# Kernel tuning notes

Hardware: AMD Instinct MI355X
Metric: run time of the kernel (lower is better)

## Reference

```python
import jax, jax.numpy as jnp
import numpy as np

N_NODES = 50000
N_EDGES = 800000  # avg degree 16
D = 16            # in_features == out_features (required by final matmul shape)


def setup_inputs() -> dict:
    key = jax.random.key(0)
    k1, k2, k3, k4 = jax.random.split(key, 4)
    x = jax.random.normal(k1, (N_NODES, D), dtype=jnp.float32)
    edge_index = jax.random.randint(k2, (2, N_EDGES), 0, N_NODES, dtype=jnp.int64)
    # shared internal weight of the (0e x 0e -> 0e, 'uvw') segmented tensor product
    W_tp = jax.random.normal(k3, (D, D, D), dtype=jnp.float32) * (1.0 / D)
    # nn.Parameter(torch.randn(out, in) * 0.01)
    weight = jax.random.normal(k4, (D, D), dtype=jnp.float32) * 0.01
    bias = jnp.zeros((D,), dtype=jnp.float32)
    return {"x": x, "edge_index": edge_index, "W_tp": W_tp, "weight": weight, "bias": bias}


def reference(x, edge_index, W_tp, weight, bias):
    # x: [N, D]; edge_index: [2, E]
    row, col = edge_index[0], edge_index[1]
    xr = x[row]  # gather source-node features   [E, D]
    xc = x[col]  # gather neighbor-node features [E, D]
    # Equivariant tensor product: with greedy irreps everything lands in 0e,
    # the only CG-allowed path is 0e x 0e -> 0e with CG coeff 1 and a shared
    # fully-connected ('uvw') weight -> per-edge bilinear form.
    messages = jnp.einsum('eu,ev,uvw->ew', xr, xc, W_tp)  # [E, D]
    # scatter-add messages back to the row nodes (index_add_)
    out = jnp.zeros((x.shape[0], D), dtype=x.dtype).at[row].add(messages)
    # dense linear: out @ weight.T + bias
    return out @ weight.T + bias
```

## Files before the change

### kernel.cpp

```cpp
#include <hip/hip_runtime.h>
#include <hip/hip_bf16.h>


#define D16 16
#define WF_STRIDE 260

__global__ __launch_bounds__(256) void fuse_w(const float* __restrict__ Wtp,
                                              const float* __restrict__ wgt,
                                              float* __restrict__ Wf) {
    int t  = blockIdx.x * 256 + threadIdx.x;
    int o  = t & 15;
    int uv = t >> 4;
    float acc = 0.f;
#pragma unroll
    for (int w = 0; w < D16; ++w)
        acc = fmaf(Wtp[uv * D16 + w], wgt[o * D16 + w], acc);
    Wf[o * WF_STRIDE + uv] = acc;
}

__global__ __launch_bounds__(256) void scatter_k(const int* __restrict__ ei,
                                                 const float* __restrict__ x,
                                                 float* __restrict__ agg,
                                                 int E) {
    int t = blockIdx.x * 256 + threadIdx.x;
    if (t >= E * D16) return;
    int e = t >> 4;
    int v = t & 15;
    int r = ei[e];
    int c = ei[E + e];
    unsafeAtomicAdd(&agg[r * D16 + v], x[c * D16 + v]);
}

__global__ __launch_bounds__(256) void bilinear_k(const float* __restrict__ x,
                                                  const float* __restrict__ agg,
                                                  const float* __restrict__ Wf,
                                                  const float* __restrict__ bias,
                                                  float* __restrict__ out,
                                                  int N) {
    __shared__ float sWf[D16 * WF_STRIDE];
    __shared__ float sx[256];
    __shared__ float sa[256];
    __shared__ float sbias[D16];

    int t = threadIdx.x;
    for (int i = t; i < D16 * WF_STRIDE; i += 256) sWf[i] = Wf[i];
    int gbase = blockIdx.x * 256;
    int g = gbase + t;
    int total = N * D16;
    if (g < total) { sx[t] = x[g]; sa[t] = agg[g]; }
    if (t < D16) sbias[t] = bias[t];
    __syncthreads();

    if (g >= total) return;
    int nl = t >> 4;
    int o  = t & 15;

    float xv[D16], av[D16];
#pragma unroll
    for (int i = 0; i < D16; ++i) {
        xv[i] = sx[nl * D16 + i];
        av[i] = sa[nl * D16 + i];
    }

    const float* wrow = &sWf[o * WF_STRIDE];
    float acc = sbias[o];
#pragma unroll
    for (int u = 0; u < D16; ++u) {
        float tu = 0.f;
#pragma unroll
        for (int v = 0; v < D16; ++v)
            tu = fmaf(av[v], wrow[u * D16 + v], tu);
        acc = fmaf(xv[u], tu, acc);
    }
    out[g] = acc;
}

extern "C" void kernel_launch(void* const* d_in, const int* in_sizes, int n_in,
                              void* d_out, int out_size, void* d_ws, size_t ws_size,
                              hipStream_t stream) {
    const float* x    = (const float*)d_in[0];
    const int*   ei   = (const int*)d_in[1];
    const float* Wtp  = (const float*)d_in[2];
    const float* wgt  = (const float*)d_in[3];
    const float* bias = (const float*)d_in[4];
    float* out = (float*)d_out;

    int N = in_sizes[0] / D16;
    int E = in_sizes[1] / 2;

    float* agg = (float*)d_ws;
    float* Wf  = agg + (size_t)N * D16;

    hipMemsetAsync(agg, 0, (size_t)N * D16 * sizeof(float), stream);

    fuse_w<<<16, 256, 0, stream>>>(Wtp, wgt, Wf);

    int sthreads = E * D16;
    scatter_k<<<(sthreads + 255) / 256, 256, 0, stream>>>(ei, x, agg, E);

    bilinear_k<<<(N * D16 + 255) / 256, 256, 0, stream>>>(x, agg, Wf, bias, out, N);
}
```

Measured before the change: 123.1 us.

## Use packed float2 atomics in scatter and fuse weight prep into bilinear kernel

The scatter kernel now handles two features per thread and issues packed v2f32 global atomic adds, halving the number of atomic operations. The separate weight-fusion kernel is removed; each bilinear block recomputes the fused weight directly into shared memory, which saves a launch but repeats that work in every block. The bilinear kernel now processes four nodes per thread so each shared-memory weight load feeds several FMAs.

Result: slower. 190.6 us (+54.9%).

```diff
diff --git a/kernel.cpp b/kernel.cpp
--- a/kernel.cpp
+++ b/kernel.cpp
@@ -4,75 +4,103 @@
 
 #define D16 16
 #define WF_STRIDE 260
+#define NT 4
+#define NB 64
 
-__global__ __launch_bounds__(256) void fuse_w(const float* __restrict__ Wtp,
-                                              const float* __restrict__ wgt,
-                                              float* __restrict__ Wf) {
-    int t  = blockIdx.x * 256 + threadIdx.x;
-    int o  = t & 15;
-    int uv = t >> 4;
-    float acc = 0.f;
-#pragma unroll
-    for (int w = 0; w < D16; ++w)
-        acc = fmaf(Wtp[uv * D16 + w], wgt[o * D16 + w], acc);
-    Wf[o * WF_STRIDE + uv] = acc;
-}
+typedef float v2f __attribute__((ext_vector_type(2)));
 
 __global__ __launch_bounds__(256) void scatter_k(const int* __restrict__ ei,
                                                  const float* __restrict__ x,
                                                  float* __restrict__ agg,
                                                  int E) {
     int t = blockIdx.x * 256 + threadIdx.x;
-    if (t >= E * D16) return;
-    int e = t >> 4;
-    int v = t & 15;
+    if (t >= E * 8) return;
+    int e = t >> 3;
+    int p = t & 7;
     int r = ei[e];
     int c = ei[E + e];
-    unsafeAtomicAdd(&agg[r * D16 + v], x[c * D16 + v]);
+    v2f val = *(const v2f*)(&x[c * D16 + p * 2]);
+#if __has_builtin(__builtin_amdgcn_global_atomic_fadd_v2f32)
+    __builtin_amdgcn_global_atomic_fadd_v2f32((v2f*)&agg[r * D16 + p * 2], val);
+#else
+    unsafeAtomicAdd(&agg[r * D16 + p * 2 + 0], val.x);
+    unsafeAtomicAdd(&agg[r * D16 + p * 2 + 1], val.y);
+#endif
 }
 
 __global__ __launch_bounds__(256) void bilinear_k(const float* __restrict__ x,
                                                   const float* __restrict__ agg,
-                                                  const float* __restrict__ Wf,
+                                                  const float* __restrict__ Wtp,
+                                                  const float* __restrict__ wgt,
                                                   const float* __restrict__ bias,
                                                   float* __restrict__ out,
                                                   int N) {
     __shared__ float sWf[D16 * WF_STRIDE];
-    __shared__ float sx[256];
-    __shared__ float sa[256];
-    __shared__ float sbias[D16];
+    __shared__ float sx[NB * D16];
+    __shared__ float sa[NB * D16];
 
     int t = threadIdx.x;
-    for (int i = t; i < D16 * WF_STRIDE; i += 256) sWf[i] = Wf[i];
-    int gbase = blockIdx.x * 256;
-    int g = gbase + t;
-    int total = N * D16;
-    if (g < total) { sx[t] = x[g]; sa[t] = agg[g]; }
-    if (t < D16) sbias[t] = bias[t];
+
+    for (int i = t; i < D16 * WF_STRIDE; i += 256) {
+        int o  = i / WF_STRIDE;
+        int uv = i - o * WF_STRIDE;
+        float acc = 0.f;
+        if (uv < 256) {
+#pragma unroll
+            for (int w = 0; w < D16; ++w)
+                acc = fmaf(Wtp[uv * D16 + w], wgt[o * D16 + w], acc);
+        }
+        sWf[i] = acc;
+    }
+
+    int nbase = blockIdx.x * NB;
+    for (int i = t; i < NB * D16; i += 256) {
+        int g = nbase * D16 + i;
+        bool ok = g < N * D16;
+        sx[i] = ok ? x[g] : 0.f;
+        sa[i] = ok ? agg[g] : 0.f;
+    }
     __syncthreads();
 
-    if (g >= total) return;
-    int nl = t >> 4;
-    int o  = t & 15;
+    int o   = t & 15;
+    int gq  = t >> 4;
+    int nl0 = gq * NT;
 
-    float xv[D16], av[D16];
+    float xv[NT][D16], av[NT][D16];
 #pragma unroll
-    for (int i = 0; i < D16; ++i) {
-        xv[i] = sx[nl * D16 + i];
-        av[i] = sa[nl * D16 + i];
+    for (int k = 0; k < NT; ++k)
+#pragma unroll
+        for (int i = 0; i < D16; ++i) {
+            xv[k][i] = sx[(nl0 + k) * D16 + i];
+            av[k][i] = sa[(nl0 + k) * D16 + i];
+        }
+
+    float b = bias[o];
+    float acc[NT];
+#pragma unroll
+    for (int k = 0; k < NT; ++k) acc[k] = b;
+
+    const float* wrow = &sWf[o * WF_STRIDE];
+#pragma unroll
+    for (int u = 0; u < D16; ++u) {
+        float tu[NT] = {0.f, 0.f, 0.f, 0.f};
+#pragma unroll
+        for (int v = 0; v < D16; ++v) {
+            float wv = wrow[u * D16 + v];
+#pragma unroll
+            for (int k = 0; k < NT; ++k)
+                tu[k] = fmaf(av[k][v], wv, tu[k]);
+        }
+#pragma unroll
+        for (int k = 0; k < NT; ++k)
+            acc[k] = fmaf(xv[k][u], tu[k], acc[k]);
     }
 
-    const float* wrow = &sWf[o * WF_STRIDE];
-    float acc = sbias[o];
 #pragma unroll
-    for (int u = 0; u < D16; ++u) {
-        float tu = 0.f;
-#pragma unroll
-        for (int v = 0; v < D16; ++v)
-            tu = fmaf(av[v], wrow[u * D16 + v], tu);
-        acc = fmaf(xv[u], tu, acc);
+    for (int k = 0; k < NT; ++k) {
+        int n = nbase + nl0 + k;
+        if (n < N) out[n * D16 + o] = acc[k];
     }
-    out[g] = acc;
 }
 
 extern "C" void kernel_launch(void* const* d_in, const int* in_sizes, int n_in,
@@ -89,14 +117,12 @@
     int E = in_sizes[1] / 2;
 
     float* agg = (float*)d_ws;
-    float* Wf  = agg + (size_t)N * D16;
 
     hipMemsetAsync(agg, 0, (size_t)N * D16 * sizeof(float), stream);
 
-    fuse_w<<<16, 256, 0, stream>>>(Wtp, wgt, Wf);
-
-    int sthreads = E * D16;
+    int sthreads = E * 8;
     scatter_k<<<(sthreads + 255) / 256, 256, 0, stream>>>(ei, x, agg, E);
 
-    bilinear_k<<<(N * D16 + 255) / 256, 256, 0, stream>>>(x, agg, Wf, bias, out, N);
+    int nblocks = (N + NB - 1) / NB;
+    bilinear_k<<<nblocks, 256, 0, stream>>>(x, agg, Wtp, wgt, bias, out, N);
 }
```
